# Kernel optimization log

Measured on AMD Instinct MI355X. Metric: run time of the kernel, lower is better.

Reference implementation:

```python
import jax, jax.numpy as jnp
import numpy as np

V = 50000      # word vocab
CV = 128       # char vocab
E = 64         # char embedding size
H = 512        # GRU hidden / word embedding size
T = 20         # max spelling length
B = 2048       # batch of words


def setup_inputs() -> dict:
    key = jax.random.key(0)
    ks = jax.random.split(key, 8)
    chars = jax.random.randint(ks[0], (V, T), 1, CV)
    lengths = jax.random.randint(ks[1], (V,), 1, T + 1)
    mask = jnp.arange(T)[None, :] < lengths[:, None]
    chars = jnp.where(mask, chars, 0)  # padding_idx = 0 beyond each length
    spelling_table = jnp.concatenate([chars, lengths[:, None]], axis=1).astype(jnp.int32)
    data = jax.random.randint(ks[2], (B,), 0, V).astype(jnp.int32)
    s = 1.0 / np.sqrt(H)
    emb = (jax.random.normal(ks[3], (CV, E), jnp.float32) * 0.1).at[0].set(0.0)
    W_ih = jax.random.uniform(ks[4], (3 * H, E), jnp.float32, -s, s)
    W_hh = jax.random.uniform(ks[5], (3 * H, H), jnp.float32, -s, s)
    b_ih = jax.random.uniform(ks[6], (3 * H,), jnp.float32, -s, s)
    b_hh = jax.random.uniform(ks[7], (3 * H,), jnp.float32, -s, s)
    return {"data": data, "spelling_table": spelling_table, "emb": emb,
            "W_ih": W_ih, "W_hh": W_hh, "b_ih": b_ih, "b_hh": b_hh}


def reference(data, spelling_table, emb, W_ih, W_hh, b_ih, b_hh):
    H_ = W_hh.shape[1]
    rec = spelling_table[data]            # [B, T+1] gather of spellings
    spelling = rec[:, :-1]                # [B, T] char ids
    lengths = rec[:, -1]                  # [B]
    # torch.sort(lengths, descending=True): stable descending argsort
    perm = jnp.argsort(-lengths)
    sorted_sp = spelling[perm]            # [B, T]
    sorted_len = lengths[perm]            # [B]
    x = emb[sorted_sp]                    # [B, T, E]
    # precompute input projections for all timesteps (fused r|z|n gates)
    xW = jnp.einsum('bte,ge->btg', x, W_ih) + b_ih   # [B, T, 3H]
    valid = (jnp.arange(x.shape[1])[None, :] < sorted_len[:, None])  # [B, T]

    def step(h, inp):
        xw_t, v_t = inp                   # [B, 3H], [B, 1]
        hW = h @ W_hh.T + b_hh            # [B, 3H]
        xr, xz, xn = jnp.split(xw_t, 3, axis=-1)
        hr, hz, hn = jnp.split(hW, 3, axis=-1)
        r = jax.nn.sigmoid(xr + hr)
        z = jax.nn.sigmoid(xz + hz)
        n = jnp.tanh(xn + r * hn)
        h_new = (1.0 - z) * n + z * h
        h = jnp.where(v_t, h_new, h)      # packed-sequence semantics
        return h, None

    h0 = jnp.zeros((x.shape[0], H_), x.dtype)
    ht, _ = jax.lax.scan(step, h0, (jnp.swapaxes(xW, 0, 1), valid.T[:, :, None]))
    # faithful reproduction of the original's unsort: ht[sorted_length_idx]
    return ht[perm]
```

## Files before the change

kernel.cpp:

```cpp
#include <hip/hip_runtime.h>
#include <hip/hip_bf16.h>
#include <math.h>

#define B_  2048
#define E_  64
#define H_  512
#define T_  20

typedef _Float16 half8 __attribute__((ext_vector_type(8)));
typedef __attribute__((ext_vector_type(4))) float f32x4;
typedef unsigned long long u64;

#define mf16(a, b, c) __builtin_amdgcn_mfma_f32_16x16x32_f16(a, b, c, 0, 0, 0)

__device__ __forceinline__ float sigmoidf_(float x) {
  return 1.0f / (1.0f + __expf(-x));
}
__device__ __forceinline__ float tanh_fast(float x) {
  float e = __expf(2.0f * x);
  return 1.0f - 2.0f / (e + 1.0f);
}

__global__ __launch_bounds__(256) void k_setup(const int* __restrict__ data,
                                               const int* __restrict__ st,
                                               int* __restrict__ perm,
                                               int* __restrict__ iperm,
                                               int* __restrict__ Mt,
                                               int* __restrict__ bar) {
  __shared__ int lens[B_];
  __shared__ int hist[256][22];
  __shared__ int sub[16][22];
  __shared__ int subpre[16][22];
  __shared__ int cnt[32];
  __shared__ int offs[32];
  int tid = threadIdx.x;

  #pragma unroll
  for (int i = 0; i < 4; ++i) bar[tid * 4 + i] = 0;

  #pragma unroll
  for (int q = 0; q < 8; ++q) {
    int i = tid * 8 + q;
    lens[i] = st[data[i] * (T_ + 1) + T_];
  }
  #pragma unroll
  for (int L = 0; L < 22; ++L) hist[tid][L] = 0;
  #pragma unroll
  for (int q = 0; q < 8; ++q) hist[tid][lens[tid * 8 + q]]++;
  __syncthreads();

  for (int q = tid; q < 16 * 21; q += 256) {
    int g = q / 21, L = q % 21;
    int run = 0;
    for (int j = 0; j < 16; ++j) {
      int v = hist[g * 16 + j][L];
      hist[g * 16 + j][L] = run;
      run += v;
    }
    sub[g][L] = run;
  }
  __syncthreads();
  if (tid < 21) {
    int run = 0;
    for (int g = 0; g < 16; ++g) { subpre[g][tid] = run; run += sub[g][tid]; }
    cnt[tid] = run;
  }
  __syncthreads();
  if (tid <= 20) {
    int s = 0;
    for (int L = tid + 1; L <= 20; ++L) s += cnt[L];
    offs[tid] = s;
  }
  __syncthreads();
  if (tid < T_) Mt[tid] = offs[tid];
  if (tid >= T_ && tid < 32) Mt[tid] = 0;

  int g = tid >> 4;
  #pragma unroll
  for (int q = 0; q < 8; ++q) {
    int i = tid * 8 + q;
    int L = lens[i];
    int rk = subpre[g][L] + hist[tid][L];
    hist[tid][L] += 1;
    perm[offs[L] + rk] = i;
  }
  __syncthreads();
  #pragma unroll
  for (int q = 0; q < 8; ++q) {
    int i = tid * 8 + q;
    iperm[perm[i]] = i;
  }
}

__global__ void k_schars(const int* __restrict__ data, const int* __restrict__ st,
                         const int* __restrict__ perm, int* __restrict__ schars_T) {
  int idx = blockIdx.x * 256 + threadIdx.x;
  if (idx >= B_ * T_) return;
  int t = idx >> 11;
  int j = idx & (B_ - 1);
  schars_T[idx] = st[data[perm[j]] * (T_ + 1) + t];
}

__global__ void k_wconv(const float* __restrict__ W_ih, const float* __restrict__ W_hh,
                        _Float16* __restrict__ Wp) {
  int idx = blockIdx.x * 256 + threadIdx.x;
  if (idx >= 8 * 18 * 12 * 512) return;
  int e = idx & 7;
  int l = (idx >> 3) & 63;
  int rest = idx >> 9;
  int g = rest % 3;  rest /= 3;
  int w = rest & 3;  rest >>= 2;
  int c = rest % 18;
  int cb = rest / 18;
  int grow = g * H_ + cb * 64 + w * 16 + (l & 15);
  int k = c * 32 + (l >> 4) * 8 + e;
  float v = (k < E_) ? W_ih[grow * E_ + k] : W_hh[grow * H_ + (k - E_)];
  Wp[idx] = (_Float16)v;
}

__global__ void k_embconv(const float* __restrict__ emb, _Float16* __restrict__ embp) {
  int idx = blockIdx.x * 256 + threadIdx.x;
  if (idx >= 128 * E_) return;
  embp[idx] = (_Float16)emb[idx];
}

__global__ __launch_bounds__(256, 1) void k_gru(
    const int* __restrict__ Mt, const int* __restrict__ schars_T,
    const _Float16* __restrict__ embp, const _Float16* __restrict__ Wp,
    const float* __restrict__ b_ih, const float* __restrict__ b_hh,
    _Float16* __restrict__ hq0, _Float16* __restrict__ hq1,
    const int* __restrict__ iperm, float* __restrict__ out,
    int* __restrict__ flags) {
  __shared__ __attribute__((aligned(16))) _Float16 As[64][512];

  int bid = blockIdx.x;
  int rb = bid & 31, cb = bid >> 5;
  int m0 = rb * 64;
  int tid = threadIdx.x;
  int w = tid >> 6, l = tid & 63;
  int ln = l & 15, kc = l >> 4;
  int rS = tid >> 2, qS = tid & 3;

  half8 wfr[54];
#define WLD(c, g) (*(const half8*)(Wp + ((((size_t)cb * 18 + (c)) * 4 + w) * 3 + (g)) * 512 + l * 8))
  #pragma unroll
  for (int g = 0; g < 3; ++g) {
    wfr[0 + g] = WLD(0, g);
    wfr[3 + g] = WLD(1, g);
    wfr[6 + g] = WLD(2 + 2 * cb, g);
    wfr[9 + g] = WLD(3 + 2 * cb, g);
  }
  #pragma unroll
  for (int jj = 0; jj < 7; ++jj) {
    int j = (cb + 1 + jj) & 7;
    #pragma unroll
    for (int c2 = 0; c2 < 2; ++c2)
      #pragma unroll
      for (int g = 0; g < 3; ++g)
        wfr[12 + jj * 6 + c2 * 3 + g] = WLD(2 + 2 * j + c2, g);
  }
#undef WLD

  int colg = cb * 64 + w * 16 + ln;
  float br  = b_ih[colg] + b_hh[colg];
  float bz  = b_ih[H_ + colg] + b_hh[H_ + colg];
  float bnx = b_ih[2 * H_ + colg];
  float bnh = b_hh[2 * H_ + colg];

  float hreg[4][4];
  #pragma unroll
  for (int i = 0; i < 4; ++i)
    #pragma unroll
    for (int j = 0; j < 4; ++j) hreg[i][j] = 0.0f;

  int myflag = rb * 8 + cb;
  int Mnext = Mt[0];

  #pragma unroll 1
  for (int t = 0; t < T_; ++t) {
    int M = Mnext;
    if (m0 >= M) break;
    Mnext = Mt[t + 1];
    const _Float16* hin  = (t & 1) ? hq1 : hq0;
    _Float16*       hout = (t & 1) ? hq0 : hq1;

    int ch[4];
    #pragma unroll
    for (int rf = 0; rf < 4; ++rf)
      ch[rf] = schars_T[t * B_ + m0 + rf * 16 + ln];

    f32x4 accr[4], accz[4], accnx[4], accnh[4];
    #pragma unroll
    for (int i = 0; i < 4; ++i) {
      accr[i] = (f32x4){0.f, 0.f, 0.f, 0.f};
      accz[i] = (f32x4){0.f, 0.f, 0.f, 0.f};
      accnx[i] = (f32x4){0.f, 0.f, 0.f, 0.f};
      accnh[i] = (f32x4){0.f, 0.f, 0.f, 0.f};
    }

    #pragma unroll
    for (int rf = 0; rf < 4; ++rf) {
      const _Float16* ep = embp + ch[rf] * E_ + kc * 8;
      half8 a0 = *(const half8*)ep;
      half8 a1 = *(const half8*)(ep + 32);
      accr[rf]  = mf16(a0, wfr[0], accr[rf]);
      accz[rf]  = mf16(a0, wfr[1], accz[rf]);
      accnx[rf] = mf16(a0, wfr[2], accnx[rf]);
      accr[rf]  = mf16(a1, wfr[3], accr[rf]);
      accz[rf]  = mf16(a1, wfr[4], accz[rf]);
      accnx[rf] = mf16(a1, wfr[5], accnx[rf]);
    }

    if (t > 0) {
      #pragma unroll
      for (int c2 = 0; c2 < 2; ++c2)
        #pragma unroll
        for (int rf = 0; rf < 4; ++rf) {
          int r = rf * 16 + ln;
          int slot = (c2 * 4 + kc) ^ (ln & 7);
          half8 af = *(const half8*)((const char*)As + r * 1024 + cb * 128 + slot * 16);
          accr[rf]  = mf16(af, wfr[6 + c2 * 3 + 0], accr[rf]);
          accz[rf]  = mf16(af, wfr[6 + c2 * 3 + 1], accz[rf]);
          accnh[rf] = mf16(af, wfr[6 + c2 * 3 + 2], accnh[rf]);
        }

      int* fb = flags + rb * 8;
      int ready = 0;
      while (!ready) {
        int acc = 1;
        #pragma unroll
        for (int jj = 0; jj < 7; ++jj) {
          int j = (cb + 1 + jj) & 7;
          int f = __hip_atomic_load(fb + j, __ATOMIC_RELAXED, __HIP_MEMORY_SCOPE_AGENT);
          acc &= (f >= t) ? 1 : 0;
        }
        ready = acc;
      }

      u64 sb[7][4];
      #pragma unroll
      for (int jj = 0; jj < 7; ++jj) {
        int j = (cb + 1 + jj) & 7;
        const u64* gp = (const u64*)(hin + (size_t)(m0 + rS) * H_ + j * 64);
        #pragma unroll
        for (int i = 0; i < 4; ++i)
          sb[jj][i] = __hip_atomic_load((u64*)(gp + qS + 4 * i),
                                        __ATOMIC_RELAXED, __HIP_MEMORY_SCOPE_AGENT);
      }

      #pragma unroll
      for (int jj = 0; jj < 7; ++jj) {
        int j = (cb + 1 + jj) & 7;
        #pragma unroll
        for (int i = 0; i < 4; ++i) {
          int u = qS + 4 * i;
          int slot = (u >> 1) ^ (rS & 7);
          *(u64*)((char*)As + rS * 1024 + j * 128 + slot * 16 + (u & 1) * 8) = sb[jj][i];
        }
        __syncthreads();
        #pragma unroll
        for (int c2 = 0; c2 < 2; ++c2)
          #pragma unroll
          for (int rf = 0; rf < 4; ++rf) {
            int r = rf * 16 + ln;
            int slot = (c2 * 4 + kc) ^ (ln & 7);
            half8 af = *(const half8*)((const char*)As + r * 1024 + j * 128 + slot * 16);
            accr[rf]  = mf16(af, wfr[12 + jj * 6 + c2 * 3 + 0], accr[rf]);
            accz[rf]  = mf16(af, wfr[12 + jj * 6 + c2 * 3 + 1], accz[rf]);
            accnh[rf] = mf16(af, wfr[12 + jj * 6 + c2 * 3 + 2], accnh[rf]);
          }
      }
    }

    #pragma unroll
    for (int rf = 0; rf < 4; ++rf) {
      #pragma unroll
      for (int q = 0; q < 4; ++q) {
        int row_l = rf * 16 + kc * 4 + q;
        if (m0 + row_l < M) {
          float r_ = sigmoidf_(accr[rf][q] + br);
          float z_ = sigmoidf_(accz[rf][q] + bz);
          float n_ = tanh_fast(accnx[rf][q] + bnx + r_ * (accnh[rf][q] + bnh));
          hreg[rf][q] = (1.0f - z_) * n_ + z_ * hreg[rf][q];
        }
        int c = w * 16 + ln;
        int slot = (c >> 3) ^ (row_l & 7);
        *(_Float16*)((char*)As + row_l * 1024 + cb * 128 + slot * 16 + (c & 7) * 2) =
            (_Float16)hreg[rf][q];
      }
    }
    __syncthreads();

    #pragma unroll
    for (int i = 0; i < 4; ++i) {
      int u = qS + 4 * i;
      int slot = (u >> 1) ^ (rS & 7);
      u64 v = *(const u64*)((const char*)As + rS * 1024 + cb * 128 + slot * 16 + (u & 1) * 8);
      __hip_atomic_store((u64*)(hout + (size_t)(m0 + rS) * H_ + cb * 64) + u, v,
                         __ATOMIC_RELAXED, __HIP_MEMORY_SCOPE_AGENT);
    }
    asm volatile("s_waitcnt vmcnt(0)" ::: "memory");
    __syncthreads();
    if (tid == 0)
      __hip_atomic_store(flags + myflag, t + 1, __ATOMIC_RELAXED, __HIP_MEMORY_SCOPE_AGENT);
  }

  #pragma unroll
  for (int rf = 0; rf < 4; ++rf) {
    #pragma unroll
    for (int q = 0; q < 4; ++q) {
      int row = m0 + rf * 16 + kc * 4 + q;
      out[(size_t)iperm[row] * H_ + colg] = hreg[rf][q];
    }
  }
}

extern "C" void kernel_launch(void* const* d_in, const int* in_sizes, int n_in,
                              void* d_out, int out_size, void* d_ws, size_t ws_size,
                              hipStream_t stream) {
  const int*   data = (const int*)d_in[0];
  const int*   st   = (const int*)d_in[1];
  const float* emb  = (const float*)d_in[2];
  const float* W_ih = (const float*)d_in[3];
  const float* W_hh = (const float*)d_in[4];
  const float* b_ih = (const float*)d_in[5];
  const float* b_hh = (const float*)d_in[6];
  float* out = (float*)d_out;

  _Float16* hq0  = (_Float16*)d_ws;
  _Float16* hq1  = hq0 + B_ * H_;
  _Float16* Wp   = hq1 + B_ * H_;
  _Float16* embp = Wp + 8 * 18 * 12 * 512;
  int* perm   = (int*)(embp + 128 * E_);
  int* iperm  = perm + B_;
  int* Mt     = iperm + B_;
  int* bar    = Mt + 32;
  int* schars = bar + 32 * 32;

  k_setup<<<1, 256, 0, stream>>>(data, st, perm, iperm, Mt, bar);
  k_schars<<<(B_ * T_ + 255) / 256, 256, 0, stream>>>(data, st, perm, schars);
  k_wconv<<<(8 * 18 * 12 * 512 + 255) / 256, 256, 0, stream>>>(W_ih, W_hh, Wp);
  k_embconv<<<(128 * E_ + 255) / 256, 256, 0, stream>>>(emb, embp);

  k_gru<<<dim3(256), dim3(256), 0, stream>>>(Mt, schars, embp, Wp, b_ih, b_hh,
                                             hq0, hq1, iperm, out, bar);
}
```

Before: 191.7 us.

## Split GRU K-reduction across two wave groups with LDS partial-sum combine

Doubles the GRU block to 512 threads and splits the 18 K-chunks of the fused input+hidden GEMM between two 4-wave halves, so each wave holds only 27 weight fragments in registers instead of 54. The second half writes its partial r/z/nh accumulators to a new LDS buffer, and the first half adds them before applying the gate nonlinearities. This is meant to halve the serial MFMA chain per wave within each timestep and relieve register pressure. In exchange it adds an extra LDS round trip and barrier every step, and more threads take part in the per-step spin synchronisation.

```diff
diff --git a/kernel.cpp b/kernel.cpp
--- a/kernel.cpp
+++ b/kernel.cpp
@@ -124,7 +124,7 @@
   embp[idx] = (_Float16)emb[idx];
 }
 
-__global__ __launch_bounds__(256, 1) void k_gru(
+__global__ __launch_bounds__(512, 1) void k_gru(
     const int* __restrict__ Mt, const int* __restrict__ schars_T,
     const _Float16* __restrict__ embp, const _Float16* __restrict__ Wp,
     const float* __restrict__ b_ih, const float* __restrict__ b_hh,
@@ -132,36 +132,28 @@
     const int* __restrict__ iperm, float* __restrict__ out,
     int* __restrict__ flags) {
   __shared__ __attribute__((aligned(16))) _Float16 As[64][512];
+  __shared__ __attribute__((aligned(16))) float Rs[4][3][64][17];
 
   int bid = blockIdx.x;
   int rb = bid & 31, cb = bid >> 5;
   int m0 = rb * 64;
   int tid = threadIdx.x;
-  int w = tid >> 6, l = tid & 63;
-  int ln = l & 15, kc = l >> 4;
-  int rS = tid >> 2, qS = tid & 3;
-
-  half8 wfr[54];
-#define WLD(c, g) (*(const half8*)(Wp + ((((size_t)cb * 18 + (c)) * 4 + w) * 3 + (g)) * 512 + l * 8))
-  #pragma unroll
-  for (int g = 0; g < 3; ++g) {
-    wfr[0 + g] = WLD(0, g);
-    wfr[3 + g] = WLD(1, g);
-    wfr[6 + g] = WLD(2 + 2 * cb, g);
-    wfr[9 + g] = WLD(3 + 2 * cb, g);
-  }
-  #pragma unroll
-  for (int jj = 0; jj < 7; ++jj) {
-    int j = (cb + 1 + jj) & 7;
-    #pragma unroll
-    for (int c2 = 0; c2 < 2; ++c2)
-      #pragma unroll
-      for (int g = 0; g < 3; ++g)
-        wfr[12 + jj * 6 + c2 * 3 + g] = WLD(2 + 2 * j + c2, g);
-  }
-#undef WLD
-
-  int colg = cb * 64 + w * 16 + ln;
+  int w = tid >> 6, kh = w >> 2, wc = w & 3;
+  int l = tid & 63, ln = l & 15, kc = l >> 4;
+  int rS = tid >> 3, uS = tid & 7;
+
+  half8 wfr[27];
+  #pragma unroll
+  for (int f = 0; f < 9; ++f) {
+    #pragma unroll
+    for (int g = 0; g < 3; ++g) {
+      int c = kh * 9 + f;
+      wfr[f * 3 + g] = *(const half8*)(
+          Wp + ((((size_t)cb * 18 + c) * 4 + wc) * 3 + g) * 512 + l * 8);
+    }
+  }
+
+  int colg = cb * 64 + wc * 16 + ln;
   float br  = b_ih[colg] + b_hh[colg];
   float bz  = b_ih[H_ + colg] + b_hh[H_ + colg];
   float bnx = b_ih[2 * H_ + colg];
@@ -175,6 +167,20 @@
 
   int myflag = rb * 8 + cb;
   int Mnext = Mt[0];
+
+#define H_CHUNK(C, F)                                                          \
+  {                                                                            \
+    const int jsl = ((C) - 2) >> 1, c2 = ((C) - 2) & 1;                        \
+    _Pragma("unroll")                                                          \
+    for (int rf = 0; rf < 4; ++rf) {                                           \
+      int r = rf * 16 + ln;                                                    \
+      int slot = (c2 * 4 + kc) ^ (ln & 7);                                     \
+      half8 af = *(const half8*)((const char*)As + r * 1024 + jsl * 128 + slot * 16); \
+      accr[rf] = mf16(af, wfr[(F) * 3 + 0], accr[rf]);                         \
+      accz[rf] = mf16(af, wfr[(F) * 3 + 1], accz[rf]);                         \
+      accnh[rf] = mf16(af, wfr[(F) * 3 + 2], accnh[rf]);                       \
+    }                                                                          \
+  }
 
   #pragma unroll 1
   for (int t = 0; t < T_; ++t) {
@@ -184,11 +190,6 @@
     const _Float16* hin  = (t & 1) ? hq1 : hq0;
     _Float16*       hout = (t & 1) ? hq0 : hq1;
 
-    int ch[4];
-    #pragma unroll
-    for (int rf = 0; rf < 4; ++rf)
-      ch[rf] = schars_T[t * B_ + m0 + rf * 16 + ln];
-
     f32x4 accr[4], accz[4], accnx[4], accnh[4];
     #pragma unroll
     for (int i = 0; i < 4; ++i) {
@@ -198,31 +199,40 @@
       accnh[i] = (f32x4){0.f, 0.f, 0.f, 0.f};
     }
 
-    #pragma unroll
-    for (int rf = 0; rf < 4; ++rf) {
-      const _Float16* ep = embp + ch[rf] * E_ + kc * 8;
-      half8 a0 = *(const half8*)ep;
-      half8 a1 = *(const half8*)(ep + 32);
-      accr[rf]  = mf16(a0, wfr[0], accr[rf]);
-      accz[rf]  = mf16(a0, wfr[1], accz[rf]);
-      accnx[rf] = mf16(a0, wfr[2], accnx[rf]);
-      accr[rf]  = mf16(a1, wfr[3], accr[rf]);
-      accz[rf]  = mf16(a1, wfr[4], accz[rf]);
-      accnx[rf] = mf16(a1, wfr[5], accnx[rf]);
+    if (kh == 0) {
+      #pragma unroll
+      for (int rf = 0; rf < 4; ++rf) {
+        int ch = schars_T[t * B_ + m0 + rf * 16 + ln];
+        const _Float16* ep = embp + ch * E_ + kc * 8;
+        half8 a0 = *(const half8*)ep;
+        half8 a1 = *(const half8*)(ep + 32);
+        accr[rf]  = mf16(a0, wfr[0], accr[rf]);
+        accz[rf]  = mf16(a0, wfr[1], accz[rf]);
+        accnx[rf] = mf16(a0, wfr[2], accnx[rf]);
+        accr[rf]  = mf16(a1, wfr[3], accr[rf]);
+        accz[rf]  = mf16(a1, wfr[4], accz[rf]);
+        accnx[rf] = mf16(a1, wfr[5], accnx[rf]);
+      }
     }
 
     if (t > 0) {
-      #pragma unroll
-      for (int c2 = 0; c2 < 2; ++c2)
-        #pragma unroll
-        for (int rf = 0; rf < 4; ++rf) {
-          int r = rf * 16 + ln;
-          int slot = (c2 * 4 + kc) ^ (ln & 7);
-          half8 af = *(const half8*)((const char*)As + r * 1024 + cb * 128 + slot * 16);
-          accr[rf]  = mf16(af, wfr[6 + c2 * 3 + 0], accr[rf]);
-          accz[rf]  = mf16(af, wfr[6 + c2 * 3 + 1], accz[rf]);
-          accnh[rf] = mf16(af, wfr[6 + c2 * 3 + 2], accnh[rf]);
-        }
+      if (kh == 0) {
+        #pragma unroll
+        for (int j = 0; j < 4; ++j) {
+          if (j == cb) {
+            H_CHUNK(2 + 2 * j, 2 + 2 * j);
+            if (3 + 2 * j <= 8) H_CHUNK(3 + 2 * j, 3 + 2 * j);
+          }
+        }
+      } else {
+        #pragma unroll
+        for (int j = 3; j < 8; ++j) {
+          if (j == cb) {
+            if (2 + 2 * j >= 9) H_CHUNK(2 + 2 * j, 2 + 2 * j - 9);
+            H_CHUNK(3 + 2 * j, 3 + 2 * j - 9);
+          }
+        }
+      }
 
       int* fb = flags + rb * 8;
       int ready = 0;
@@ -237,66 +247,82 @@
         ready = acc;
       }
 
-      u64 sb[7][4];
-      #pragma unroll
-      for (int jj = 0; jj < 7; ++jj) {
-        int j = (cb + 1 + jj) & 7;
-        const u64* gp = (const u64*)(hin + (size_t)(m0 + rS) * H_ + j * 64);
-        #pragma unroll
-        for (int i = 0; i < 4; ++i)
-          sb[jj][i] = __hip_atomic_load((u64*)(gp + qS + 4 * i),
-                                        __ATOMIC_RELAXED, __HIP_MEMORY_SCOPE_AGENT);
-      }
-
-      #pragma unroll
-      for (int jj = 0; jj < 7; ++jj) {
-        int j = (cb + 1 + jj) & 7;
-        #pragma unroll
-        for (int i = 0; i < 4; ++i) {
-          int u = qS + 4 * i;
+      u64 sb[8][2];
+      #pragma unroll
+      for (int j = 0; j < 8; ++j) {
+        if (j != cb) {
+          const u64* gp = (const u64*)(hin + (size_t)(m0 + rS) * H_) + j * 16;
+          sb[j][0] = __hip_atomic_load((u64*)(gp + uS),
+                                       __ATOMIC_RELAXED, __HIP_MEMORY_SCOPE_AGENT);
+          sb[j][1] = __hip_atomic_load((u64*)(gp + uS + 8),
+                                       __ATOMIC_RELAXED, __HIP_MEMORY_SCOPE_AGENT);
+        }
+      }
+
+      #pragma unroll
+      for (int j = 0; j < 8; ++j) {
+        if (j == cb) continue;
+        #pragma unroll
+        for (int i = 0; i < 2; ++i) {
+          int u = uS + 8 * i;
           int slot = (u >> 1) ^ (rS & 7);
-          *(u64*)((char*)As + rS * 1024 + j * 128 + slot * 16 + (u & 1) * 8) = sb[jj][i];
+          *(u64*)((char*)As + rS * 1024 + j * 128 + slot * 16 + (u & 1) * 8) = sb[j][i];
         }
         __syncthreads();
-        #pragma unroll
-        for (int c2 = 0; c2 < 2; ++c2)
-          #pragma unroll
-          for (int rf = 0; rf < 4; ++rf) {
-            int r = rf * 16 + ln;
-            int slot = (c2 * 4 + kc) ^ (ln & 7);
-            half8 af = *(const half8*)((const char*)As + r * 1024 + j * 128 + slot * 16);
-            accr[rf]  = mf16(af, wfr[12 + jj * 6 + c2 * 3 + 0], accr[rf]);
-            accz[rf]  = mf16(af, wfr[12 + jj * 6 + c2 * 3 + 1], accz[rf]);
-            accnh[rf] = mf16(af, wfr[12 + jj * 6 + c2 * 3 + 2], accnh[rf]);
+        if (kh == 0) {
+          if (2 + 2 * j <= 8) H_CHUNK(2 + 2 * j, 2 + 2 * j);
+          if (3 + 2 * j <= 8) H_CHUNK(3 + 2 * j, 3 + 2 * j);
+        } else {
+          if (2 + 2 * j >= 9) H_CHUNK(2 + 2 * j, 2 + 2 * j - 9);
+          if (3 + 2 * j >= 9) H_CHUNK(3 + 2 * j, 3 + 2 * j - 9);
+        }
+      }
+    }
+
+    if (kh == 1) {
+      #pragma unroll
+      for (int rf = 0; rf < 4; ++rf)
+        #pragma unroll
+        for (int q = 0; q < 4; ++q) {
+          int row = rf * 16 + kc * 4 + q;
+          Rs[wc][0][row][ln] = accr[rf][q];
+          Rs[wc][1][row][ln] = accz[rf][q];
+          Rs[wc][2][row][ln] = accnh[rf][q];
+        }
+    }
+    __syncthreads();
+
+    if (kh == 0) {
+      #pragma unroll
+      for (int rf = 0; rf < 4; ++rf) {
+        #pragma unroll
+        for (int q = 0; q < 4; ++q) {
+          int row_l = rf * 16 + kc * 4 + q;
+          if (m0 + row_l < M) {
+            float pr = accr[rf][q] + Rs[wc][0][row_l][ln] + br;
+            float pz = accz[rf][q] + Rs[wc][1][row_l][ln] + bz;
+            float xn = accnx[rf][q] + bnx;
+            float hn = accnh[rf][q] + Rs[wc][2][row_l][ln] + bnh;
+            float r_ = sigmoidf_(pr);
+            float z_ = sigmoidf_(pz);
+            float n_ = tanh_fast(xn + r_ * hn);
+            hreg[rf][q] = (1.0f - z_) * n_ + z_ * hreg[rf][q];
           }
-      }
-    }
-
-    #pragma unroll
-    for (int rf = 0; rf < 4; ++rf) {
-      #pragma unroll
-      for (int q = 0; q < 4; ++q) {
-        int row_l = rf * 16 + kc * 4 + q;
-        if (m0 + row_l < M) {
-          float r_ = sigmoidf_(accr[rf][q] + br);
-          float z_ = sigmoidf_(accz[rf][q] + bz);
-          float n_ = tanh_fast(accnx[rf][q] + bnx + r_ * (accnh[rf][q] + bnh));
-          hreg[rf][q] = (1.0f - z_) * n_ + z_ * hreg[rf][q];
-        }
-        int c = w * 16 + ln;
-        int slot = (c >> 3) ^ (row_l & 7);
-        *(_Float16*)((char*)As + row_l * 1024 + cb * 128 + slot * 16 + (c & 7) * 2) =
-            (_Float16)hreg[rf][q];
+          int c = wc * 16 + ln;
+          int slot = (c >> 3) ^ (row_l & 7);
+          *(_Float16*)((char*)As + row_l * 1024 + cb * 128 + slot * 16 + (c & 7) * 2) =
+              (_Float16)hreg[rf][q];
+        }
       }
     }
     __syncthreads();
 
     #pragma unroll
-    for (int i = 0; i < 4; ++i) {
-      int u = qS + 4 * i;
+    for (int i = 0; i < 2; ++i) {
+      int u = uS + 8 * i;
       int slot = (u >> 1) ^ (rS & 7);
       u64 v = *(const u64*)((const char*)As + rS * 1024 + cb * 128 + slot * 16 + (u & 1) * 8);
-      __hip_atomic_store((u64*)(hout + (size_t)(m0 + rS) * H_ + cb * 64) + u, v,
+      __hip_atomic_store((u64*)(hout + (size_t)(m0 + rS) * H_) + cb * 16 + u, v,
                          __ATOMIC_RELAXED, __HIP_MEMORY_SCOPE_AGENT);
     }
     asm volatile("s_waitcnt vmcnt(0)" ::: "memory");
@@ -304,13 +330,16 @@
     if (tid == 0)
       __hip_atomic_store(flags + myflag, t + 1, __ATOMIC_RELAXED, __HIP_MEMORY_SCOPE_AGENT);
   }
-
-  #pragma unroll
-  for (int rf = 0; rf < 4; ++rf) {
-    #pragma unroll
-    for (int q = 0; q < 4; ++q) {
-      int row = m0 + rf * 16 + kc * 4 + q;
-      out[(size_t)iperm[row] * H_ + colg] = hreg[rf][q];
+#undef H_CHUNK
+
+  if (kh == 0) {
+    #pragma unroll
+    for (int rf = 0; rf < 4; ++rf) {
+      #pragma unroll
+      for (int q = 0; q < 4; ++q) {
+        int row = m0 + rf * 16 + kc * 4 + q;
+        out[(size_t)iperm[row] * H_ + colg] = hreg[rf][q];
+      }
     }
   }
 }
@@ -342,6 +371,6 @@
   k_wconv<<<(8 * 18 * 12 * 512 + 255) / 256, 256, 0, stream>>>(W_ih, W_hh, Wp);
   k_embconv<<<(128 * E_ + 255) / 256, 256, 0, stream>>>(emb, embp);
 
-  k_gru<<<dim3(256), dim3(256), 0, stream>>>(Mt, schars, embp, Wp, b_ih, b_hh,
+  k_gru<<<dim3(256), dim3(512), 0, stream>>>(Mt, schars, embp, Wp, b_ih, b_hh,
                                              hq0, hq1, iperm, out, bar);
 }
```

Result: slower. 274.4 us (+43.1%).

## Precompute char-vocab input projection table and split GRU into 512 blocks

Applied to the files above, without the earlier changes.

Replaces the per-step MFMA input projection with a precomputed 128x3H table (emb@W_ih^T plus biases), so each step just gathers three floats per output. The persistent GRU kernel now uses 32-row tiles across 512 blocks at two blocks per CU. Part of the W_hh fragments is held in registers and the rest in shared memory. The flag polling is done by a single thread followed by a block barrier. This trades fewer MFMAs and more parallelism for scattered global gathers of the table, more LDS traffic for weights, and twice as many blocks in the cross-block flag synchronisation.

```diff
diff --git a/kernel.cpp b/kernel.cpp
--- a/kernel.cpp
+++ b/kernel.cpp
@@ -26,7 +26,7 @@
                                                int* __restrict__ perm,
                                                int* __restrict__ iperm,
                                                int* __restrict__ Mt,
-                                               int* __restrict__ bar) {
+                                               int* __restrict__ flags) {
   __shared__ int lens[B_];
   __shared__ int hist[256][22];
   __shared__ int sub[16][22];
@@ -36,7 +36,7 @@
   int tid = threadIdx.x;
 
   #pragma unroll
-  for (int i = 0; i < 4; ++i) bar[tid * 4 + i] = 0;
+  for (int i = 0; i < 4; ++i) flags[tid * 4 + i] = 0;
 
   #pragma unroll
   for (int q = 0; q < 8; ++q) {
@@ -101,80 +101,101 @@
   schars_T[idx] = st[data[perm[j]] * (T_ + 1) + t];
 }
 
-__global__ void k_wconv(const float* __restrict__ W_ih, const float* __restrict__ W_hh,
-                        _Float16* __restrict__ Wp) {
+__global__ void k_wconv(const float* __restrict__ W_hh, _Float16* __restrict__ Wp) {
   int idx = blockIdx.x * 256 + threadIdx.x;
-  if (idx >= 8 * 18 * 12 * 512) return;
+  if (idx >= 8 * 16 * 12 * 512) return;
   int e = idx & 7;
   int l = (idx >> 3) & 63;
   int rest = idx >> 9;
   int g = rest % 3;  rest /= 3;
-  int w = rest & 3;  rest >>= 2;
-  int c = rest % 18;
-  int cb = rest / 18;
-  int grow = g * H_ + cb * 64 + w * 16 + (l & 15);
+  int wc = rest & 3; rest >>= 2;
+  int c = rest % 16;
+  int cb = rest / 16;
+  int grow = g * H_ + cb * 64 + wc * 16 + (l & 15);
   int k = c * 32 + (l >> 4) * 8 + e;
-  float v = (k < E_) ? W_ih[grow * E_ + k] : W_hh[grow * H_ + (k - E_)];
-  Wp[idx] = (_Float16)v;
-}
-
-__global__ void k_embconv(const float* __restrict__ emb, _Float16* __restrict__ embp) {
-  int idx = blockIdx.x * 256 + threadIdx.x;
-  if (idx >= 128 * E_) return;
-  embp[idx] = (_Float16)emb[idx];
-}
-
-__global__ __launch_bounds__(256, 1) void k_gru(
+  Wp[idx] = (_Float16)W_hh[grow * H_ + k];
+}
+
+__global__ __launch_bounds__(256) void k_embw(const float* __restrict__ emb,
+                                              const float* __restrict__ W_ih,
+                                              const float* __restrict__ b_ih,
+                                              const float* __restrict__ b_hh,
+                                              float* __restrict__ embW) {
+  int c = blockIdx.x;
+  int tid = threadIdx.x;
+  __shared__ float ev[64];
+  if (tid < 64) ev[tid] = emb[c * E_ + tid];
+  __syncthreads();
+  for (int o = tid; o < 3 * H_; o += 256) {
+    float s = b_ih[o];
+    if (o < 2 * H_) s += b_hh[o];
+    #pragma unroll
+    for (int k = 0; k < E_; ++k) s = fmaf(ev[k], W_ih[o * E_ + k], s);
+    embW[(size_t)c * (3 * H_) + o] = s;
+  }
+}
+
+__global__ __launch_bounds__(256, 2) void k_gru(
     const int* __restrict__ Mt, const int* __restrict__ schars_T,
-    const _Float16* __restrict__ embp, const _Float16* __restrict__ Wp,
-    const float* __restrict__ b_ih, const float* __restrict__ b_hh,
+    const float* __restrict__ embW, const _Float16* __restrict__ Wp,
+    const float* __restrict__ b_hh,
     _Float16* __restrict__ hq0, _Float16* __restrict__ hq1,
     const int* __restrict__ iperm, float* __restrict__ out,
     int* __restrict__ flags) {
-  __shared__ __attribute__((aligned(16))) _Float16 As[64][512];
+  __shared__ __attribute__((aligned(16))) _Float16 As[32][512];
+  __shared__ __attribute__((aligned(16))) _Float16 Ws[3 * 12 * 512];
 
   int bid = blockIdx.x;
-  int rb = bid & 31, cb = bid >> 5;
-  int m0 = rb * 64;
+  int rb = bid >> 3, cb = bid & 7;
+  int m0 = rb * 32;
   int tid = threadIdx.x;
-  int w = tid >> 6, l = tid & 63;
-  int ln = l & 15, kc = l >> 4;
-  int rS = tid >> 2, qS = tid & 3;
-
-  half8 wfr[54];
-#define WLD(c, g) (*(const half8*)(Wp + ((((size_t)cb * 18 + (c)) * 4 + w) * 3 + (g)) * 512 + l * 8))
-  #pragma unroll
-  for (int g = 0; g < 3; ++g) {
-    wfr[0 + g] = WLD(0, g);
-    wfr[3 + g] = WLD(1, g);
-    wfr[6 + g] = WLD(2 + 2 * cb, g);
-    wfr[9 + g] = WLD(3 + 2 * cb, g);
-  }
-  #pragma unroll
-  for (int jj = 0; jj < 7; ++jj) {
-    int j = (cb + 1 + jj) & 7;
-    #pragma unroll
-    for (int c2 = 0; c2 < 2; ++c2)
-      #pragma unroll
-      for (int g = 0; g < 3; ++g)
-        wfr[12 + jj * 6 + c2 * 3 + g] = WLD(2 + 2 * j + c2, g);
-  }
-#undef WLD
+  int w = tid >> 6;
+  int l = tid & 63, ln = l & 15, kc = l >> 4;
+  int rS = tid >> 3, uS = tid & 7;
+
+  {
+    const uint4* src = (const uint4*)(Wp + ((size_t)(cb * 16 + 13) * 12) * 512);
+    uint4* dst = (uint4*)Ws;
+    #pragma unroll
+    for (int i = 0; i < 9; ++i) dst[tid + 256 * i] = src[tid + 256 * i];
+  }
+
+  half8 wfr[39];
+  #pragma unroll
+  for (int c = 0; c < 13; ++c)
+    #pragma unroll
+    for (int g = 0; g < 3; ++g)
+      wfr[c * 3 + g] = *(const half8*)(
+          Wp + (((size_t)(cb * 16 + c) * 4 + w) * 3 + g) * 512 + l * 8);
+  __syncthreads();
 
   int colg = cb * 64 + w * 16 + ln;
-  float br  = b_ih[colg] + b_hh[colg];
-  float bz  = b_ih[H_ + colg] + b_hh[H_ + colg];
-  float bnx = b_ih[2 * H_ + colg];
   float bnh = b_hh[2 * H_ + colg];
 
-  float hreg[4][4];
-  #pragma unroll
-  for (int i = 0; i < 4; ++i)
+  float hreg[2][4];
+  #pragma unroll
+  for (int i = 0; i < 2; ++i)
     #pragma unroll
     for (int j = 0; j < 4; ++j) hreg[i][j] = 0.0f;
 
-  int myflag = rb * 8 + cb;
   int Mnext = Mt[0];
+
+#define WFRAG(c, g) ((c) < 13 ? wfr[(c) * 3 + (g)]                            \
+    : *(const half8*)(Ws + (((c) - 13) * 12 + w * 3 + (g)) * 512 + l * 8))
+
+#define H_CHUNK(c)                                                             \
+  {                                                                            \
+    const int jsl = (c) >> 1, c2 = (c) & 1;                                    \
+    _Pragma("unroll")                                                          \
+    for (int rf = 0; rf < 2; ++rf) {                                           \
+      int r = rf * 16 + ln;                                                    \
+      int slot = (c2 * 4 + kc) ^ (ln & 7);                                     \
+      half8 af = *(const half8*)((const char*)As + r * 1024 + jsl * 128 + slot * 16); \
+      accr[rf]  = mf16(af, WFRAG(c, 0), accr[rf]);                             \
+      accz[rf]  = mf16(af, WFRAG(c, 1), accz[rf]);                             \
+      accnh[rf] = mf16(af, WFRAG(c, 2), accnh[rf]);                            \
+    }                                                                          \
+  }
 
   #pragma unroll 1
   for (int t = 0; t < T_; ++t) {
@@ -184,103 +205,81 @@
     const _Float16* hin  = (t & 1) ? hq1 : hq0;
     _Float16*       hout = (t & 1) ? hq0 : hq1;
 
-    int ch[4];
-    #pragma unroll
-    for (int rf = 0; rf < 4; ++rf)
-      ch[rf] = schars_T[t * B_ + m0 + rf * 16 + ln];
-
-    f32x4 accr[4], accz[4], accnx[4], accnh[4];
-    #pragma unroll
-    for (int i = 0; i < 4; ++i) {
+    int chv[2][4];
+    #pragma unroll
+    for (int rf = 0; rf < 2; ++rf)
+      #pragma unroll
+      for (int q = 0; q < 4; ++q)
+        chv[rf][q] = schars_T[t * B_ + m0 + rf * 16 + kc * 4 + q];
+
+    f32x4 accr[2], accz[2], accnh[2];
+    #pragma unroll
+    for (int i = 0; i < 2; ++i) {
       accr[i] = (f32x4){0.f, 0.f, 0.f, 0.f};
       accz[i] = (f32x4){0.f, 0.f, 0.f, 0.f};
-      accnx[i] = (f32x4){0.f, 0.f, 0.f, 0.f};
       accnh[i] = (f32x4){0.f, 0.f, 0.f, 0.f};
     }
 
-    #pragma unroll
-    for (int rf = 0; rf < 4; ++rf) {
-      const _Float16* ep = embp + ch[rf] * E_ + kc * 8;
-      half8 a0 = *(const half8*)ep;
-      half8 a1 = *(const half8*)(ep + 32);
-      accr[rf]  = mf16(a0, wfr[0], accr[rf]);
-      accz[rf]  = mf16(a0, wfr[1], accz[rf]);
-      accnx[rf] = mf16(a0, wfr[2], accnx[rf]);
-      accr[rf]  = mf16(a1, wfr[3], accr[rf]);
-      accz[rf]  = mf16(a1, wfr[4], accz[rf]);
-      accnx[rf] = mf16(a1, wfr[5], accnx[rf]);
-    }
-
     if (t > 0) {
       #pragma unroll
-      for (int c2 = 0; c2 < 2; ++c2)
-        #pragma unroll
-        for (int rf = 0; rf < 4; ++rf) {
-          int r = rf * 16 + ln;
-          int slot = (c2 * 4 + kc) ^ (ln & 7);
-          half8 af = *(const half8*)((const char*)As + r * 1024 + cb * 128 + slot * 16);
-          accr[rf]  = mf16(af, wfr[6 + c2 * 3 + 0], accr[rf]);
-          accz[rf]  = mf16(af, wfr[6 + c2 * 3 + 1], accz[rf]);
-          accnh[rf] = mf16(af, wfr[6 + c2 * 3 + 2], accnh[rf]);
+      for (int j = 0; j < 8; ++j)
+        if (j == cb) { H_CHUNK(2 * j) H_CHUNK(2 * j + 1) }
+
+      if (tid == 0) {
+        int* fb = flags + rb * 16;
+        int ready = 0;
+        while (!ready) {
+          int acc = 1;
+          #pragma unroll
+          for (int j = 0; j < 8; ++j) {
+            if (j == cb) continue;
+            int f = __hip_atomic_load(fb + j, __ATOMIC_RELAXED, __HIP_MEMORY_SCOPE_AGENT);
+            acc &= (f >= t) ? 1 : 0;
+          }
+          ready = acc;
         }
-
-      int* fb = flags + rb * 8;
-      int ready = 0;
-      while (!ready) {
-        int acc = 1;
-        #pragma unroll
-        for (int jj = 0; jj < 7; ++jj) {
-          int j = (cb + 1 + jj) & 7;
-          int f = __hip_atomic_load(fb + j, __ATOMIC_RELAXED, __HIP_MEMORY_SCOPE_AGENT);
-          acc &= (f >= t) ? 1 : 0;
+      }
+      __syncthreads();
+
+      u64 sb[8][2];
+      #pragma unroll
+      for (int j = 0; j < 8; ++j) {
+        if (j != cb) {
+          const u64* gp = (const u64*)(hin + (size_t)(m0 + rS) * H_ + j * 64);
+          sb[j][0] = __hip_atomic_load((u64*)(gp + uS * 2),
+                                       __ATOMIC_RELAXED, __HIP_MEMORY_SCOPE_AGENT);
+          sb[j][1] = __hip_atomic_load((u64*)(gp + uS * 2 + 1),
+                                       __ATOMIC_RELAXED, __HIP_MEMORY_SCOPE_AGENT);
         }
-        ready = acc;
       }
 
-      u64 sb[7][4];
-      #pragma unroll
-      for (int jj = 0; jj < 7; ++jj) {
-        int j = (cb + 1 + jj) & 7;
-        const u64* gp = (const u64*)(hin + (size_t)(m0 + rS) * H_ + j * 64);
-        #pragma unroll
-        for (int i = 0; i < 4; ++i)
-          sb[jj][i] = __hip_atomic_load((u64*)(gp + qS + 4 * i),
-                                        __ATOMIC_RELAXED, __HIP_MEMORY_SCOPE_AGENT);
-      }
-
-      #pragma unroll
-      for (int jj = 0; jj < 7; ++jj) {
-        int j = (cb + 1 + jj) & 7;
-        #pragma unroll
-        for (int i = 0; i < 4; ++i) {
-          int u = qS + 4 * i;
-          int slot = (u >> 1) ^ (rS & 7);
-          *(u64*)((char*)As + rS * 1024 + j * 128 + slot * 16 + (u & 1) * 8) = sb[jj][i];
+      #pragma unroll
+      for (int j = 0; j < 8; ++j) {
+        if (j == cb) continue;
+        {
+          char* dp = (char*)As + rS * 1024 + j * 128 + ((uS ^ (rS & 7)) * 16);
+          ((u64*)dp)[0] = sb[j][0];
+          ((u64*)dp)[1] = sb[j][1];
         }
         __syncthreads();
-        #pragma unroll
-        for (int c2 = 0; c2 < 2; ++c2)
-          #pragma unroll
-          for (int rf = 0; rf < 4; ++rf) {
-            int r = rf * 16 + ln;
-            int slot = (c2 * 4 + kc) ^ (ln & 7);
-            half8 af = *(const half8*)((const char*)As + r * 1024 + j * 128 + slot * 16);
-            accr[rf]  = mf16(af, wfr[12 + jj * 6 + c2 * 3 + 0], accr[rf]);
-            accz[rf]  = mf16(af, wfr[12 + jj * 6 + c2 * 3 + 1], accz[rf]);
-            accnh[rf] = mf16(af, wfr[12 + jj * 6 + c2 * 3 + 2], accnh[rf]);
-          }
+        H_CHUNK(2 * j)
+        H_CHUNK(2 * j + 1)
       }
     }
 
     #pragma unroll
-    for (int rf = 0; rf < 4; ++rf) {
+    for (int rf = 0; rf < 2; ++rf) {
       #pragma unroll
       for (int q = 0; q < 4; ++q) {
         int row_l = rf * 16 + kc * 4 + q;
         if (m0 + row_l < M) {
-          float r_ = sigmoidf_(accr[rf][q] + br);
-          float z_ = sigmoidf_(accz[rf][q] + bz);
-          float n_ = tanh_fast(accnx[rf][q] + bnx + r_ * (accnh[rf][q] + bnh));
+          const float* ew = embW + (size_t)chv[rf][q] * (3 * H_) + colg;
+          float xwr = ew[0];
+          float xwz = ew[H_];
+          float xwn = ew[2 * H_];
+          float r_ = sigmoidf_(accr[rf][q] + xwr);
+          float z_ = sigmoidf_(accz[rf][q] + xwz);
+          float n_ = tanh_fast(xwn + r_ * (accnh[rf][q] + bnh));
           hreg[rf][q] = (1.0f - z_) * n_ + z_ * hreg[rf][q];
         }
         int c = w * 16 + ln;
@@ -291,22 +290,25 @@
     }
     __syncthreads();
 
-    #pragma unroll
-    for (int i = 0; i < 4; ++i) {
-      int u = qS + 4 * i;
-      int slot = (u >> 1) ^ (rS & 7);
-      u64 v = *(const u64*)((const char*)As + rS * 1024 + cb * 128 + slot * 16 + (u & 1) * 8);
-      __hip_atomic_store((u64*)(hout + (size_t)(m0 + rS) * H_ + cb * 64) + u, v,
-                         __ATOMIC_RELAXED, __HIP_MEMORY_SCOPE_AGENT);
+    {
+      const char* sp = (const char*)As + rS * 1024 + cb * 128 + ((uS ^ (rS & 7)) * 16);
+      u64 v0 = ((const u64*)sp)[0];
+      u64 v1 = ((const u64*)sp)[1];
+      u64* gp = (u64*)(hout + (size_t)(m0 + rS) * H_ + cb * 64);
+      __hip_atomic_store(gp + uS * 2, v0, __ATOMIC_RELAXED, __HIP_MEMORY_SCOPE_AGENT);
+      __hip_atomic_store(gp + uS * 2 + 1, v1, __ATOMIC_RELAXED, __HIP_MEMORY_SCOPE_AGENT);
     }
     asm volatile("s_waitcnt vmcnt(0)" ::: "memory");
     __syncthreads();
     if (tid == 0)
-      __hip_atomic_store(flags + myflag, t + 1, __ATOMIC_RELAXED, __HIP_MEMORY_SCOPE_AGENT);
-  }
-
-  #pragma unroll
-  for (int rf = 0; rf < 4; ++rf) {
+      __hip_atomic_store(flags + rb * 16 + cb, t + 1,
+                         __ATOMIC_RELAXED, __HIP_MEMORY_SCOPE_AGENT);
+  }
+#undef H_CHUNK
+#undef WFRAG
+
+  #pragma unroll
+  for (int rf = 0; rf < 2; ++rf) {
     #pragma unroll
     for (int q = 0; q < 4; ++q) {
       int row = m0 + rf * 16 + kc * 4 + q;
@@ -330,18 +332,18 @@
   _Float16* hq0  = (_Float16*)d_ws;
   _Float16* hq1  = hq0 + B_ * H_;
   _Float16* Wp   = hq1 + B_ * H_;
-  _Float16* embp = Wp + 8 * 18 * 12 * 512;
-  int* perm   = (int*)(embp + 128 * E_);
+  float*    embW = (float*)(Wp + 8 * 16 * 12 * 512);
+  int* perm   = (int*)(embW + 128 * 3 * H_);
   int* iperm  = perm + B_;
   int* Mt     = iperm + B_;
-  int* bar    = Mt + 32;
-  int* schars = bar + 32 * 32;
-
-  k_setup<<<1, 256, 0, stream>>>(data, st, perm, iperm, Mt, bar);
+  int* flags  = Mt + 32;
+  int* schars = flags + 64 * 16;
+
+  k_setup<<<1, 256, 0, stream>>>(data, st, perm, iperm, Mt, flags);
   k_schars<<<(B_ * T_ + 255) / 256, 256, 0, stream>>>(data, st, perm, schars);
-  k_wconv<<<(8 * 18 * 12 * 512 + 255) / 256, 256, 0, stream>>>(W_ih, W_hh, Wp);
-  k_embconv<<<(128 * E_ + 255) / 256, 256, 0, stream>>>(emb, embp);
-
-  k_gru<<<dim3(256), dim3(256), 0, stream>>>(Mt, schars, embp, Wp, b_ih, b_hh,
-                                             hq0, hq1, iperm, out, bar);
-}
+  k_wconv<<<(8 * 16 * 12 * 512 + 255) / 256, 256, 0, stream>>>(W_hh, Wp);
+  k_embw<<<128, 256, 0, stream>>>(emb, W_ih, b_ih, b_hh, embW);
+
+  k_gru<<<dim3(512), dim3(256), 0, stream>>>(Mt, schars, embW, Wp, b_hh,
+                                             hq0, hq1, iperm, out, flags);
+}
```

Measured after the change: 226.3 us. +18.0%, slower.
